# Kernel tuning notes

Measured on AMD Instinct MI355X. Metric: run time of the kernel, lower is better.

The kernel has to match this reference:

```python
import jax, jax.numpy as jnp
import numpy as np

N, E, R = 50000, 800000, 3
IN_DIM, HID_DIM, OUT_DIM = 128, 128, 128


def setup_inputs() -> dict:
    key = jax.random.key(0)
    ks = jax.random.split(key, 16)

    def p(k, shape, scale=0.1):
        return jax.random.normal(k, shape, dtype=jnp.float32) * scale

    return {
        "x": jax.random.normal(ks[0], (N, IN_DIM), dtype=jnp.float32),
        "edge_index": jax.random.randint(ks[1], (2, E), 0, N, dtype=jnp.int32),
        "edge_type": jax.random.randint(ks[2], (E,), 0, R, dtype=jnp.int32),
        "edge_attr": jax.random.normal(ks[3], (E, 1), dtype=jnp.float32),
        # layer 1 params (RGATConv: heads=1, dim=1 -> q,k,e are [F,1])
        "w1": p(ks[4], (R, IN_DIM, HID_DIM)),
        "q1": p(ks[5], (HID_DIM, 1)),
        "k1": p(ks[6], (HID_DIM, 1)),
        "e1": p(ks[7], (HID_DIM, 1)),
        "we1": p(ks[8], (1, HID_DIM)),  # lin_edge weight (edge_dim=1 -> F), no bias
        "b1": jnp.zeros((HID_DIM,), jnp.float32),
        # layer 2 params
        "w2": p(ks[9], (R, HID_DIM, OUT_DIM)),
        "q2": p(ks[10], (OUT_DIM, 1)),
        "k2": p(ks[11], (OUT_DIM, 1)),
        "e2": p(ks[12], (OUT_DIM, 1)),
        "we2": p(ks[13], (1, OUT_DIM)),
        "b2": jnp.zeros((OUT_DIM,), jnp.float32),
    }


def _rgat_layer(x, src, dst, etype, edge_attr, w, q, k, e, we, b, num_nodes):
    """One RGATConv layer (heads=1, dim=1, additive-self-attention,
    across-relation softmax, aggr='add', concat=True)."""
    # per-node, per-relation transform: [N, R, F]
    xw = jnp.einsum('ni,rio->nro', x, w)
    # node-level attention logits per relation (cheaper than per-edge matmul)
    nq = jnp.einsum('nro,od->nrd', xw, q)  # [N, R, 1]
    nk = jnp.einsum('nro,od->nrd', xw, k)  # [N, R, 1]
    qi = nq[dst, etype]                    # [E, 1]
    kj = nk[src, etype]                    # [E, 1]
    ae = (edge_attr @ we) @ e              # lin_edge(edge_attr) @ e -> [E, 1]
    alpha = jax.nn.leaky_relu(qi + kj + ae, negative_slope=0.2)
    # segment softmax over destination nodes (PyG softmax: detached max, +1e-16)
    amax = jax.lax.stop_gradient(
        jax.ops.segment_max(alpha, dst, num_segments=num_nodes))
    ex = jnp.exp(alpha - amax[dst])
    denom = jax.ops.segment_sum(ex, dst, num_segments=num_nodes) + 1e-16
    attn = ex / denom[dst]                 # [E, 1]
    msg = attn * xw[src, etype]            # [E, F]
    out = jax.ops.segment_sum(msg, dst, num_segments=num_nodes)  # [N, F]
    return out + b


def reference(x, edge_index, edge_type, edge_attr,
              w1, q1, k1, e1, we1, b1,
              w2, q2, k2, e2, we2, b2):
    src, dst = edge_index[0], edge_index[1]
    n = x.shape[0]
    h = jax.nn.relu(_rgat_layer(x, src, dst, edge_type, edge_attr,
                                w1, q1, k1, e1, we1, b1, n))
    return _rgat_layer(h, src, dst, edge_type, edge_attr,
                       w2, q2, k2, e2, we2, b2, n)
```

## Files before the change

kernel.cpp:

```cpp
#include <hip/hip_runtime.h>

#define DIM 128

typedef __attribute__((ext_vector_type(8))) short short8;
typedef __attribute__((ext_vector_type(4))) float f32x4;

__device__ inline float bf2f(unsigned short u) {
    union { unsigned int i; float f; } v; v.i = (unsigned int)u << 16; return v.f;
}
__device__ inline unsigned short f2bf(float f) {
    union { float f; unsigned int i; } v; v.f = f;
    return (unsigned short)((v.i + 0x7FFF + ((v.i >> 16) & 1)) >> 16);
}

__global__ void precompute_k(const float* __restrict__ w1, const float* __restrict__ q1,
                             const float* __restrict__ k1, const float* __restrict__ e1,
                             const float* __restrict__ we1,
                             const float* __restrict__ w2, const float* __restrict__ q2,
                             const float* __restrict__ k2, const float* __restrict__ e2,
                             const float* __restrict__ we2,
                             float* __restrict__ wqk,
                             float* __restrict__ cc)
{
    int b = blockIdx.x;
    int i = threadIdx.x;
    if (b < 12) {
        int layer = b / 6;
        int rem   = b % 6;
        int which = rem / 3;
        int r     = rem % 3;
        const float* w = layer ? w2 : w1;
        const float* v = layer ? (which ? k2 : q2) : (which ? k1 : q1);
        const float* row = w + (r * DIM + i) * DIM;
        float s = 0.f;
#pragma unroll 8
        for (int o = 0; o < DIM; ++o) s += row[o] * v[o];
        wqk[((layer * 2 + which) * 3 + r) * DIM + i] = s;
    } else {
        if (i < 2) {
            const float* we = i ? we2 : we1;
            const float* e  = i ? e2  : e1;
            float s = 0.f;
            for (int f = 0; f < DIM; ++f) s += we[f] * e[f];
            cc[i] = s;
        }
    }
}

__global__ __launch_bounds__(256) void xconv_k(const float* __restrict__ x,
                                               unsigned short* __restrict__ xbf, int total4)
{
    int i = blockIdx.x * 256 + threadIdx.x;
    if (i >= total4) return;
    float4 v = *(const float4*)(x + (size_t)i * 4);
    unsigned short o0 = f2bf(v.x), o1 = f2bf(v.y), o2 = f2bf(v.z), o3 = f2bf(v.w);
    unsigned long long pk = (unsigned long long)o0 | ((unsigned long long)o1 << 16)
                          | ((unsigned long long)o2 << 32) | ((unsigned long long)o3 << 48);
    *(unsigned long long*)(xbf + (size_t)i * 4) = pk;
}

__global__ void wconv_k(const float* __restrict__ w1, const float* __restrict__ w2,
                        unsigned short* __restrict__ Bf)
{
    int b = blockIdx.x;
    int lane = threadIdx.x;
    int layer = b / 96;
    int rem   = b % 96;
    int ks = rem / 8, f = rem % 8;
    const float* w = layer ? w2 : w1;
    int col  = f * 16 + (lane & 15);
    int krow = ks * 32 + (lane >> 4) * 8;
    unsigned short tmp[8];
#pragma unroll
    for (int j = 0; j < 8; ++j) tmp[j] = f2bf(w[(size_t)(krow + j) * 128 + col]);
    unsigned long long* dst = (unsigned long long*)(Bf + ((size_t)b * 64 + lane) * 8);
    dst[0] = *(unsigned long long*)&tmp[0];
    dst[1] = *(unsigned long long*)&tmp[4];
}

__global__ __launch_bounds__(256) void logits_k(const unsigned short* __restrict__ xbf,
    const float* __restrict__ wq, const float* __restrict__ wk,
    float* __restrict__ nq3, float* __restrict__ nk3, int N)
{
    int lane = threadIdx.x & 63;
    int n = blockIdx.x * 4 + (threadIdx.x >> 6);
    if (n >= N) return;
    unsigned int xv = *(const unsigned int*)(xbf + (size_t)n * DIM + lane * 2);
    float x0 = bf2f((unsigned short)(xv & 0xFFFF));
    float x1 = bf2f((unsigned short)(xv >> 16));
#pragma unroll
    for (int r = 0; r < 3; ++r) {
        float2 qv = *(const float2*)(wq + r * DIM + lane * 2);
        float2 kv = *(const float2*)(wk + r * DIM + lane * 2);
        float dq = x0 * qv.x + x1 * qv.y;
        float dk = x0 * kv.x + x1 * kv.y;
#pragma unroll
        for (int off = 32; off > 0; off >>= 1) {
            dq += __shfl_xor(dq, off);
            dk += __shfl_xor(dk, off);
        }
        if (lane == 0) { nq3[n * 3 + r] = dq; nk3[n * 3 + r] = dk; }
    }
}

__global__ void hist_k(const int* __restrict__ dst, const int* __restrict__ et,
                       int* __restrict__ hist3, int E)
{
    int e = blockIdx.x * blockDim.x + threadIdx.x;
    if (e < E) atomicAdd(&hist3[dst[e] * 3 + et[e]], 1);
}

__global__ void scan1_k(const int* __restrict__ hist, int* __restrict__ bsum, int N)
{
    __shared__ int ws[4];
    int i = blockIdx.x * 256 + threadIdx.x;
    int v = (i < N) ? hist[i] : 0;
#pragma unroll
    for (int off = 32; off > 0; off >>= 1) v += __shfl_xor(v, off);
    if ((threadIdx.x & 63) == 0) ws[threadIdx.x >> 6] = v;
    __syncthreads();
    if (threadIdx.x == 0) bsum[blockIdx.x] = ws[0] + ws[1] + ws[2] + ws[3];
}

__global__ void scan2_k(const int* __restrict__ bsum, int* __restrict__ boff,
                        int* __restrict__ totalp, int nb)
{
    int lane = threadIdx.x;
    int running = 0;
    for (int base = 0; base < nb; base += 64) {
        int i = base + lane;
        int v = (i < nb) ? bsum[i] : 0;
        int s = v;
#pragma unroll
        for (int off = 1; off < 64; off <<= 1) {
            int t = __shfl_up(s, off);
            if (lane >= off) s += t;
        }
        if (i < nb) boff[i] = running + (s - v);
        running += __shfl(s, 63);
    }
    if (lane == 0) *totalp = running;
}

__global__ void scan3_k(const int* __restrict__ hist, const int* __restrict__ boff,
                        int* __restrict__ rowstart, int N)
{
    __shared__ int ws[4];
    int tid = threadIdx.x, lane = tid & 63, w = tid >> 6;
    int i = blockIdx.x * 256 + tid;
    int v = (i < N) ? hist[i] : 0;
    int s = v;
#pragma unroll
    for (int off = 1; off < 64; off <<= 1) {
        int t = __shfl_up(s, off);
        if (lane >= off) s += t;
    }
    if (lane == 63) ws[w] = s;
    __syncthreads();
    int woff = 0;
    for (int k = 0; k < w; ++k) woff += ws[k];
    if (i < N) rowstart[i] = boff[blockIdx.x] + woff + (s - v);
}

__global__ void fill_k(const int* __restrict__ src, const int* __restrict__ dst,
                       const int* __restrict__ et, const float* __restrict__ ea,
                       const int* __restrict__ rowstart3,
                       int* __restrict__ cursor3, int* __restrict__ packed,
                       float* __restrict__ ea_s, int* __restrict__ dst_s, int E)
{
    int e = blockIdx.x * blockDim.x + threadIdx.x;
    if (e >= E) return;
    int d = dst[e], t = et[e];
    int b3 = d * 3 + t;
    int pos = atomicAdd(&cursor3[b3], 1);
    int slot = rowstart3[b3] + pos;
    packed[slot] = src[e];
    ea_s[slot] = ea[e];
    dst_s[slot] = d;
}

__global__ __launch_bounds__(256) void edgeex_k(const int* __restrict__ packed,
    const float* __restrict__ ea_s, const int* __restrict__ dst_s,
    const int* __restrict__ rowstart3,
    const float* __restrict__ nq3, const float* __restrict__ nk3,
    const float* __restrict__ cc, int cidx,
    float* __restrict__ ex_s, int E)
{
    int sl = blockIdx.x * 256 + threadIdx.x;
    if (sl >= E) return;
    int srcn = packed[sl];
    int d    = dst_s[sl];
    int b3 = d * 3;
    int t = (sl >= rowstart3[b3 + 1]) + (sl >= rowstart3[b3 + 2]);
    float z = nq3[b3 + t] + nk3[srcn * 3 + t] + ea_s[sl] * cc[cidx];
    float a = z > 0.f ? z : 0.2f * z;
    ex_s[sl] = __expf(a);
}

__global__ __launch_bounds__(256) void agg_k(const unsigned short* __restrict__ xbf,
    const int* __restrict__ packed, const float* __restrict__ ex_s,
    const int* __restrict__ rowstart3,
    unsigned short* __restrict__ aggbf, int N)
{
    int tid  = threadIdx.x;
    int lane = tid & 63;
    int n = blockIdx.x * 4 + (tid >> 6);
    if (n >= N) return;
    int q  = lane >> 4;
    int fl = lane & 15;
    int b3 = n * 3;
    int rs0 = rowstart3[b3 + 0], rs1 = rowstart3[b3 + 1];
    int rs2 = rowstart3[b3 + 2], rs3 = rowstart3[b3 + 3];
    float den = 0.f;
    float a0[8], a1[8], a2[8];
#pragma unroll
    for (int j = 0; j < 8; ++j) { a0[j] = 0.f; a1[j] = 0.f; a2[j] = 0.f; }
    const unsigned short* xq = xbf + fl * 8;

#define SEG(S, E_, ACC)                                                     \
    for (int i = (S); i < (E_); i += 4) {                                   \
        int sl = i + q;                                                     \
        bool act = sl < (E_);                                               \
        sl = act ? sl : (E_) - 1;                                           \
        float ex = act ? ex_s[sl] : 0.f;                                    \
        int srcn = packed[sl];                                              \
        short8 xv = *(const short8*)(xq + (size_t)srcn * DIM);              \
        den += ex;                                                          \
        _Pragma("unroll")                                                   \
        for (int j = 0; j < 8; ++j)                                         \
            ACC[j] += ex * bf2f((unsigned short)xv[j]);                     \
    }

    SEG(rs0, rs1, a0)
    SEG(rs1, rs2, a1)
    SEG(rs2, rs3, a2)
#undef SEG

#pragma unroll
    for (int j = 0; j < 8; ++j) {
        a0[j] += __shfl_xor(a0[j], 16); a0[j] += __shfl_xor(a0[j], 32);
        a1[j] += __shfl_xor(a1[j], 16); a1[j] += __shfl_xor(a1[j], 32);
        a2[j] += __shfl_xor(a2[j], 16); a2[j] += __shfl_xor(a2[j], 32);
    }
    den += __shfl_xor(den, 16);
    den += __shfl_xor(den, 32);
    float inv = 1.f / (den + 1e-16f);

    if (q == 0) {
        unsigned short* dp = aggbf + (size_t)n * 384 + fl * 8;
#define PACKSTORE(A, OFF)                                                   \
        {                                                                   \
            unsigned int w0 = (unsigned int)f2bf(A[0] * inv) |              \
                              ((unsigned int)f2bf(A[1] * inv) << 16);       \
            unsigned int w1 = (unsigned int)f2bf(A[2] * inv) |              \
                              ((unsigned int)f2bf(A[3] * inv) << 16);       \
            unsigned int w2 = (unsigned int)f2bf(A[4] * inv) |              \
                              ((unsigned int)f2bf(A[5] * inv) << 16);       \
            unsigned int w3 = (unsigned int)f2bf(A[6] * inv) |              \
                              ((unsigned int)f2bf(A[7] * inv) << 16);       \
            uint4 u; u.x = w0; u.y = w1; u.z = w2; u.w = w3;                \
            *(uint4*)(dp + (OFF)) = u;                                      \
        }
        PACKSTORE(a0, 0)
        PACKSTORE(a1, 128)
        PACKSTORE(a2, 256)
#undef PACKSTORE
    }
}

template <int RELU>
__global__ __launch_bounds__(256) void gemm_mfma_k(const unsigned short* __restrict__ A,
    const unsigned short* __restrict__ Bf, const float* __restrict__ bias,
    unsigned short* __restrict__ hbf, float* __restrict__ out, int M)
{
    int wid  = threadIdx.x >> 6;
    int lane = threadIdx.x & 63;
    int mrow = blockIdx.x * 64 + wid * 16 + (lane & 15);
    int kl   = (lane >> 4) * 8;
    f32x4 acc[8];
#pragma unroll
    for (int f = 0; f < 8; ++f) acc[f] = (f32x4){0.f, 0.f, 0.f, 0.f};
    const unsigned short* arow = A + (size_t)mrow * 384 + kl;
    for (int ks = 0; ks < 12; ++ks) {
        short8 af = *(const short8*)(arow + ks * 32);
        const short8* bp = (const short8*)(Bf + ((size_t)(ks * 8) * 64 + lane) * 8);
#pragma unroll
        for (int f = 0; f < 8; ++f) {
            short8 bfr = bp[f * 64];
            acc[f] = __builtin_amdgcn_mfma_f32_16x16x32_bf16(af, bfr, acc[f], 0, 0, 0);
        }
    }
    int r0  = blockIdx.x * 64 + wid * 16 + (lane >> 4) * 4;
    int cl  = lane & 15;
#pragma unroll
    for (int f = 0; f < 8; ++f) {
        int col = f * 16 + cl;
        float bv = bias[col];
#pragma unroll
        for (int j = 0; j < 4; ++j) {
            int row = r0 + j;
            if (row < M) {
                float v = acc[f][j] + bv;
                if (RELU) {
                    v = v > 0.f ? v : 0.f;
                    hbf[(size_t)row * 128 + col] = f2bf(v);
                } else {
                    out[(size_t)row * 128 + col] = v;
                }
            }
        }
    }
}

extern "C" void kernel_launch(void* const* d_in, const int* in_sizes, int n_in,
                              void* d_out, int out_size, void* d_ws, size_t ws_size,
                              hipStream_t stream)
{
    const float* x   = (const float*)d_in[0];
    const int*   ei  = (const int*)d_in[1];
    const int*   etp = (const int*)d_in[2];
    const float* ea  = (const float*)d_in[3];
    const float* w1  = (const float*)d_in[4];
    const float* q1  = (const float*)d_in[5];
    const float* k1  = (const float*)d_in[6];
    const float* e1  = (const float*)d_in[7];
    const float* we1 = (const float*)d_in[8];
    const float* b1  = (const float*)d_in[9];
    const float* w2  = (const float*)d_in[10];
    const float* q2  = (const float*)d_in[11];
    const float* k2  = (const float*)d_in[12];
    const float* e2  = (const float*)d_in[13];
    const float* we2 = (const float*)d_in[14];
    const float* b2  = (const float*)d_in[15];
    float* out = (float*)d_out;

    const int N = in_sizes[0] / DIM;
    const int E = in_sizes[2];
    const int N3 = N * 3;
    const int* srcp = ei;
    const int* dstp = ei + E;

    int mb64 = (N + 63) / 64;
    int Mpad = mb64 * 64;

    char* base = (char*)d_ws;
    size_t off = 0;
    auto alloc = [&](size_t bytes) -> char* {
        char* p = base + off;
        off = (off + bytes + 255) & ~(size_t)255;
        return p;
    };
    int*   hist3   = (int*)  alloc((size_t)N3 * 4);
    int*   cursor3 = (int*)  alloc((size_t)N3 * 4);
    size_t zero_end = off;
    int*   rowstart3 = (int*)alloc((size_t)(N3 + 1) * 4);
    int*   bsum    = (int*)  alloc(1024 * 4);
    int*   boff    = (int*)  alloc(1024 * 4);
    float* wqk     = (float*)alloc(1536 * 4);
    float* cc      = (float*)alloc(2 * 4);
    float* nq3     = (float*)alloc((size_t)N * 3 * 4);
    float* nk3     = (float*)alloc((size_t)N * 3 * 4);
    int*   packed  = (int*)  alloc((size_t)E * 4);
    float* ea_s    = (float*)alloc((size_t)E * 4);
    int*   dst_s   = (int*)  alloc((size_t)E * 4);
    float* ex_s    = (float*)alloc((size_t)E * 4);
    unsigned short* xbf   = (unsigned short*)alloc((size_t)N * DIM * 2);
    unsigned short* hbf   = (unsigned short*)alloc((size_t)N * DIM * 2);
    unsigned short* aggbf = (unsigned short*)alloc((size_t)Mpad * 384 * 2);
    unsigned short* Bf    = (unsigned short*)alloc((size_t)2 * 96 * 64 * 8 * 2);
    (void)ws_size; (void)n_in; (void)out_size;

    hipMemsetAsync(base, 0, zero_end, stream);
    precompute_k<<<13, 128, 0, stream>>>(w1, q1, k1, e1, we1,
                                         w2, q2, k2, e2, we2, wqk, cc);
    int eb  = (E + 255) / 256;
    int nb4 = (N + 3) / 4;
    int sb3 = (N3 + 255) / 256;
    int total4 = N * DIM / 4;

    xconv_k<<<(total4 + 255) / 256, 256, 0, stream>>>(x, xbf, total4);
    wconv_k<<<192, 64, 0, stream>>>(w1, w2, Bf);

    hist_k<<<eb, 256, 0, stream>>>(dstp, etp, hist3, E);
    scan1_k<<<sb3, 256, 0, stream>>>(hist3, bsum, N3);
    scan2_k<<<1, 64, 0, stream>>>(bsum, boff, rowstart3 + N3, sb3);
    scan3_k<<<sb3, 256, 0, stream>>>(hist3, boff, rowstart3, N3);
    fill_k<<<eb, 256, 0, stream>>>(srcp, dstp, etp, ea, rowstart3, cursor3,
                                   packed, ea_s, dst_s, E);

    const unsigned short* Bf2 = Bf + (size_t)96 * 64 * 8;

    logits_k<<<nb4, 256, 0, stream>>>(xbf, wqk + 0, wqk + 384, nq3, nk3, N);
    edgeex_k<<<eb, 256, 0, stream>>>(packed, ea_s, dst_s, rowstart3, nq3, nk3, cc, 0, ex_s, E);
    agg_k<<<nb4, 256, 0, stream>>>(xbf, packed, ex_s, rowstart3, aggbf, N);
    gemm_mfma_k<1><<<mb64, 256, 0, stream>>>(aggbf, Bf, b1, hbf, nullptr, N);

    logits_k<<<nb4, 256, 0, stream>>>(hbf, wqk + 768, wqk + 1152, nq3, nk3, N);
    edgeex_k<<<eb, 256, 0, stream>>>(packed, ea_s, dst_s, rowstart3, nq3, nk3, cc, 1, ex_s, E);
    agg_k<<<nb4, 256, 0, stream>>>(hbf, packed, ex_s, rowstart3, aggbf, N);
    gemm_mfma_k<0><<<mb64, 256, 0, stream>>>(aggbf, Bf2, b2, nullptr, out, N);
}
```

Measured before the change: 413.0 us.

## Fuse x bf16 conversion into layer-1 logits and pack edge payload into u64

Drops the separate x-to-bf16 kernel by converting x inside a new logits kernel that also writes xbf, saving one launch and one full pass over x. Edge data (src, type, dst, bf16 edge_attr) is bit-packed into a single 64-bit word per sorted edge, replacing three separate arrays. This removes the rowstart lookups in edgeex. It adds a wider 8-byte load in agg_k where only the source index is needed. Edge_attr is also rounded to bf16, and packing assumes node ids fit in 17 bits.

```diff
diff --git a/kernel.cpp b/kernel.cpp
--- a/kernel.cpp
+++ b/kernel.cpp
@@ -4,6 +4,7 @@
 
 typedef __attribute__((ext_vector_type(8))) short short8;
 typedef __attribute__((ext_vector_type(4))) float f32x4;
+typedef unsigned long long u64;
 
 __device__ inline float bf2f(unsigned short u) {
     union { unsigned int i; float f; } v; v.i = (unsigned int)u << 16; return v.f;
@@ -47,18 +48,6 @@
     }
 }
 
-__global__ __launch_bounds__(256) void xconv_k(const float* __restrict__ x,
-                                               unsigned short* __restrict__ xbf, int total4)
-{
-    int i = blockIdx.x * 256 + threadIdx.x;
-    if (i >= total4) return;
-    float4 v = *(const float4*)(x + (size_t)i * 4);
-    unsigned short o0 = f2bf(v.x), o1 = f2bf(v.y), o2 = f2bf(v.z), o3 = f2bf(v.w);
-    unsigned long long pk = (unsigned long long)o0 | ((unsigned long long)o1 << 16)
-                          | ((unsigned long long)o2 << 32) | ((unsigned long long)o3 << 48);
-    *(unsigned long long*)(xbf + (size_t)i * 4) = pk;
-}
-
 __global__ void wconv_k(const float* __restrict__ w1, const float* __restrict__ w2,
                         unsigned short* __restrict__ Bf)
 {
@@ -73,9 +62,37 @@
     unsigned short tmp[8];
 #pragma unroll
     for (int j = 0; j < 8; ++j) tmp[j] = f2bf(w[(size_t)(krow + j) * 128 + col]);
-    unsigned long long* dst = (unsigned long long*)(Bf + ((size_t)b * 64 + lane) * 8);
-    dst[0] = *(unsigned long long*)&tmp[0];
-    dst[1] = *(unsigned long long*)&tmp[4];
+    u64* dst = (u64*)(Bf + ((size_t)b * 64 + lane) * 8);
+    dst[0] = *(u64*)&tmp[0];
+    dst[1] = *(u64*)&tmp[4];
+}
+
+__global__ __launch_bounds__(256) void xlogits_k(const float* __restrict__ x,
+    const float* __restrict__ wq, const float* __restrict__ wk,
+    unsigned short* __restrict__ xbf,
+    float* __restrict__ nq3, float* __restrict__ nk3, int N)
+{
+    int lane = threadIdx.x & 63;
+    int n = blockIdx.x * 4 + (threadIdx.x >> 6);
+    if (n >= N) return;
+    float2 xv2 = *(const float2*)(x + (size_t)n * DIM + lane * 2);
+    unsigned short o0 = f2bf(xv2.x), o1 = f2bf(xv2.y);
+    *(unsigned int*)(xbf + (size_t)n * DIM + lane * 2) =
+        (unsigned int)o0 | ((unsigned int)o1 << 16);
+    float x0 = bf2f(o0), x1 = bf2f(o1);
+#pragma unroll
+    for (int r = 0; r < 3; ++r) {
+        float2 qv = *(const float2*)(wq + r * DIM + lane * 2);
+        float2 kv = *(const float2*)(wk + r * DIM + lane * 2);
+        float dq = x0 * qv.x + x1 * qv.y;
+        float dk = x0 * kv.x + x1 * kv.y;
+#pragma unroll
+        for (int off = 32; off > 0; off >>= 1) {
+            dq += __shfl_xor(dq, off);
+            dk += __shfl_xor(dk, off);
+        }
+        if (lane == 0) { nq3[n * 3 + r] = dq; nk3[n * 3 + r] = dk; }
+    }
 }
 
 __global__ __launch_bounds__(256) void logits_k(const unsigned short* __restrict__ xbf,
@@ -165,8 +182,7 @@
 __global__ void fill_k(const int* __restrict__ src, const int* __restrict__ dst,
                        const int* __restrict__ et, const float* __restrict__ ea,
                        const int* __restrict__ rowstart3,
-                       int* __restrict__ cursor3, int* __restrict__ packed,
-                       float* __restrict__ ea_s, int* __restrict__ dst_s, int E)
+                       int* __restrict__ cursor3, u64* __restrict__ pay, int E)
 {
     int e = blockIdx.x * blockDim.x + threadIdx.x;
     if (e >= E) return;
@@ -174,31 +190,30 @@
     int b3 = d * 3 + t;
     int pos = atomicAdd(&cursor3[b3], 1);
     int slot = rowstart3[b3] + pos;
-    packed[slot] = src[e];
-    ea_s[slot] = ea[e];
-    dst_s[slot] = d;
-}
-
-__global__ __launch_bounds__(256) void edgeex_k(const int* __restrict__ packed,
-    const float* __restrict__ ea_s, const int* __restrict__ dst_s,
-    const int* __restrict__ rowstart3,
+    u64 p = (u64)(unsigned)src[e] | ((u64)(unsigned)t << 17)
+          | ((u64)(unsigned)d << 19) | ((u64)f2bf(ea[e]) << 48);
+    pay[slot] = p;
+}
+
+__global__ __launch_bounds__(256) void edgeex_k(const u64* __restrict__ pay,
     const float* __restrict__ nq3, const float* __restrict__ nk3,
     const float* __restrict__ cc, int cidx,
     float* __restrict__ ex_s, int E)
 {
     int sl = blockIdx.x * 256 + threadIdx.x;
     if (sl >= E) return;
-    int srcn = packed[sl];
-    int d    = dst_s[sl];
-    int b3 = d * 3;
-    int t = (sl >= rowstart3[b3 + 1]) + (sl >= rowstart3[b3 + 2]);
-    float z = nq3[b3 + t] + nk3[srcn * 3 + t] + ea_s[sl] * cc[cidx];
+    u64 p = pay[sl];
+    int srcn = (int)(p & 0x1FFFF);
+    int t    = (int)((p >> 17) & 3);
+    int d    = (int)((p >> 19) & 0x1FFFF);
+    float eav = bf2f((unsigned short)(p >> 48));
+    float z = nq3[d * 3 + t] + nk3[srcn * 3 + t] + eav * cc[cidx];
     float a = z > 0.f ? z : 0.2f * z;
     ex_s[sl] = __expf(a);
 }
 
 __global__ __launch_bounds__(256) void agg_k(const unsigned short* __restrict__ xbf,
-    const int* __restrict__ packed, const float* __restrict__ ex_s,
+    const u64* __restrict__ pay, const float* __restrict__ ex_s,
     const int* __restrict__ rowstart3,
     unsigned short* __restrict__ aggbf, int N)
 {
@@ -223,7 +238,7 @@
         bool act = sl < (E_);                                               \
         sl = act ? sl : (E_) - 1;                                           \
         float ex = act ? ex_s[sl] : 0.f;                                    \
-        int srcn = packed[sl];                                              \
+        int srcn = (int)(pay[sl] & 0x1FFFF);                                \
         short8 xv = *(const short8*)(xq + (size_t)srcn * DIM);              \
         den += ex;                                                          \
         _Pragma("unroll")                                                   \
@@ -360,9 +375,7 @@
     float* cc      = (float*)alloc(2 * 4);
     float* nq3     = (float*)alloc((size_t)N * 3 * 4);
     float* nk3     = (float*)alloc((size_t)N * 3 * 4);
-    int*   packed  = (int*)  alloc((size_t)E * 4);
-    float* ea_s    = (float*)alloc((size_t)E * 4);
-    int*   dst_s   = (int*)  alloc((size_t)E * 4);
+    u64*   pay     = (u64*)  alloc((size_t)E * 8);
     float* ex_s    = (float*)alloc((size_t)E * 4);
     unsigned short* xbf   = (unsigned short*)alloc((size_t)N * DIM * 2);
     unsigned short* hbf   = (unsigned short*)alloc((size_t)N * DIM * 2);
@@ -376,27 +389,24 @@
     int eb  = (E + 255) / 256;
     int nb4 = (N + 3) / 4;
     int sb3 = (N3 + 255) / 256;
-    int total4 = N * DIM / 4;
-
-    xconv_k<<<(total4 + 255) / 256, 256, 0, stream>>>(x, xbf, total4);
+
     wconv_k<<<192, 64, 0, stream>>>(w1, w2, Bf);
 
     hist_k<<<eb, 256, 0, stream>>>(dstp, etp, hist3, E);
     scan1_k<<<sb3, 256, 0, stream>>>(hist3, bsum, N3);
     scan2_k<<<1, 64, 0, stream>>>(bsum, boff, rowstart3 + N3, sb3);
     scan3_k<<<sb3, 256, 0, stream>>>(hist3, boff, rowstart3, N3);
-    fill_k<<<eb, 256, 0, stream>>>(srcp, dstp, etp, ea, rowstart3, cursor3,
-                                   packed, ea_s, dst_s, E);
+    fill_k<<<eb, 256, 0, stream>>>(srcp, dstp, etp, ea, rowstart3, cursor3, pay, E);
 
     const unsigned short* Bf2 = Bf + (size_t)96 * 64 * 8;
 
-    logits_k<<<nb4, 256, 0, stream>>>(xbf, wqk + 0, wqk + 384, nq3, nk3, N);
-    edgeex_k<<<eb, 256, 0, stream>>>(packed, ea_s, dst_s, rowstart3, nq3, nk3, cc, 0, ex_s, E);
-    agg_k<<<nb4, 256, 0, stream>>>(xbf, packed, ex_s, rowstart3, aggbf, N);
+    xlogits_k<<<nb4, 256, 0, stream>>>(x, wqk + 0, wqk + 384, xbf, nq3, nk3, N);
+    edgeex_k<<<eb, 256, 0, stream>>>(pay, nq3, nk3, cc, 0, ex_s, E);
+    agg_k<<<nb4, 256, 0, stream>>>(xbf, pay, ex_s, rowstart3, aggbf, N);
     gemm_mfma_k<1><<<mb64, 256, 0, stream>>>(aggbf, Bf, b1, hbf, nullptr, N);
 
     logits_k<<<nb4, 256, 0, stream>>>(hbf, wqk + 768, wqk + 1152, nq3, nk3, N);
-    edgeex_k<<<eb, 256, 0, stream>>>(packed, ea_s, dst_s, rowstart3, nq3, nk3, cc, 1, ex_s, E);
-    agg_k<<<nb4, 256, 0, stream>>>(hbf, packed, ex_s, rowstart3, aggbf, N);
+    edgeex_k<<<eb, 256, 0, stream>>>(pay, nq3, nk3, cc, 1, ex_s, E);
+    agg_k<<<nb4, 256, 0, stream>>>(hbf, pay, ex_s, rowstart3, aggbf, N);
     gemm_mfma_k<0><<<mb64, 256, 0, stream>>>(aggbf, Bf2, b2, nullptr, out, N);
 }
```

Result: faster. 398.7 us (-3.5%).
